# Performance work log

Measured on AMD Instinct MI355X. Metric: run time of the kernel, lower is better.

Reference implementation:

```python
import jax, jax.numpy as jnp
import numpy as np

H = 16
DH = 64  # n_state // n_head = 1024 // 16
EPS = 1e-6


def phi(x):
    return jax.nn.silu(x) + 1.0


def setup_inputs() -> dict:
    key = jax.random.key(0)
    ks = jax.random.split(key, 9)
    B, C, Tq, Tk = 8, 1024, 1500, 1500
    s = 1.0 / np.sqrt(C).astype(np.float32)
    return {
        "x": jax.random.normal(ks[0], (B, C, Tq, 1), jnp.float32),
        "xa": jax.random.normal(ks[1], (B, C, Tk, 1), jnp.float32),
        "Wq": jax.random.normal(ks[2], (C, C), jnp.float32) * s,
        "bq": jax.random.normal(ks[3], (C,), jnp.float32) * s,
        "Wk": jax.random.normal(ks[4], (C, C), jnp.float32) * s,
        "Wv": jax.random.normal(ks[5], (C, C), jnp.float32) * s,
        "bv": jax.random.normal(ks[6], (C,), jnp.float32) * s,
        "Wo": jax.random.normal(ks[7], (C, C), jnp.float32) * s,
        "bo": jax.random.normal(ks[8], (C,), jnp.float32) * s,
    }


def reference(x, xa, Wq, bq, Wk, Wv, bv, Wo, bo):
    # x: (B,C,Tq,1), xa: (B,C,Tk,1). 1x1 conv2d == matmul over channel dim.
    xq = x[..., 0]   # (B,C,Tq)
    xk = xa[..., 0]  # (B,C,Tk)
    q = jnp.einsum('oc,bct->bot', Wq, xq) + bq[None, :, None]
    k = jnp.einsum('oc,bct->bot', Wk, xk)  # key has no bias
    v = jnp.einsum('oc,bct->bot', Wv, xk) + bv[None, :, None]

    B, C, Tq = q.shape
    Tk = k.shape[2]
    pq = phi(q).reshape(B, H, DH, Tq)
    pk = phi(k).reshape(B, H, DH, Tk)
    vv = v.reshape(B, H, DH, Tk)

    k_sum = pk.sum(axis=3)            # (B,H,Dh) : sum_t phi(k)
    kv_sum = (pk * vv).sum(axis=3)    # (B,H,Dh) : diagonal phi(k)*v sum (as in source)
    den = jnp.einsum('bhdt,bhd->bht', pq, k_sum) + EPS  # (B,H,Tq)

    out = pq * kv_sum[..., None] / den[:, :, None, :]   # (B,H,Dh,Tq)
    out = out.reshape(B, C, Tq) / jnp.sqrt(jnp.asarray(DH, out.dtype))
    y = jnp.einsum('oc,bct->bot', Wo, out) + bo[None, :, None]
    return y[..., None]  # (B,C,Tq,1)
```

## Files before the change

### kernel.cpp

```cpp
#include <hip/hip_runtime.h>

typedef __attribute__((ext_vector_type(4))) float  f32x4;
typedef __attribute__((ext_vector_type(4))) float  float4v;
typedef __attribute__((ext_vector_type(8))) short  short8;
typedef __attribute__((ext_vector_type(4))) short  short4v;

#define TQ 1500
#define TP 1536
#define CC 1024
#define EPS 1e-6f

#define XT_OFF    ((size_t)0)
#define XAT_OFF   ((size_t)25165824)
#define PQT_OFF   ((size_t)50331648)
#define WB_OFF    ((size_t)75497472)
#define KSUM_OFF  ((size_t)83886080)
#define KVSUM_OFF ((size_t)83918848)
#define IDEN_OFF  ((size_t)83951616)

__device__ __forceinline__ float bf2f(short s) {
    union { unsigned u; float f; } v; v.u = ((unsigned)(unsigned short)s) << 16; return v.f;
}
__device__ __forceinline__ short f2bf(float f) {
    union { float f; unsigned u; } v; v.f = f;
    unsigned r = (v.u + 0x7FFFu + ((v.u >> 16) & 1u)) >> 16;
    return (short)r;
}
__device__ __forceinline__ float phi_f(float x) {
    return x / (1.f + __expf(-x)) + 1.f;
}
__device__ __forceinline__ void gl_lds16(const void* g, void* l) {
    __builtin_amdgcn_global_load_lds((const __attribute__((address_space(1))) void*)g,
                                     (__attribute__((address_space(3))) void*)l, 16, 0, 0);
}

__global__ __launch_bounds__(256)
void conv_w_kernel(const float* __restrict__ w0, const float* __restrict__ w1,
                   const float* __restrict__ w2, const float* __restrict__ w3,
                   short* __restrict__ o0, short* __restrict__ o1,
                   short* __restrict__ o2, short* __restrict__ o3)
{
    const int i = (blockIdx.x * 256 + threadIdx.x) * 4;
    float4v a = *(const float4v*)(w0 + i);
    float4v b = *(const float4v*)(w1 + i);
    float4v c = *(const float4v*)(w2 + i);
    float4v d = *(const float4v*)(w3 + i);
    short4v ra, rb, rc, rd;
#pragma unroll
    for (int j = 0; j < 4; ++j) {
        ra[j] = f2bf(a[j]); rb[j] = f2bf(b[j]); rc[j] = f2bf(c[j]); rd[j] = f2bf(d[j]);
    }
    *(short4v*)(o0 + i) = ra;
    *(short4v*)(o1 + i) = rb;
    *(short4v*)(o2 + i) = rc;
    *(short4v*)(o3 + i) = rd;
}

__global__ __launch_bounds__(256)
void xpose_kernel(const float* __restrict__ x, short* __restrict__ xT)
{
    __shared__ float tile[64][65];
    const int b  = blockIdx.z;
    const int c0 = blockIdx.y * 64;
    const int t0 = blockIdx.x * 64;
    const int tl = threadIdx.x & 63;
    const int q  = threadIdx.x >> 6;
    const int t  = t0 + tl;
#pragma unroll
    for (int i = 0; i < 16; ++i) {
        const int cl = q * 16 + i;
        float v = 0.f;
        if (t < TQ) v = x[((size_t)b * CC + c0 + cl) * TQ + t];
        tile[cl][tl] = v;
    }
    __syncthreads();
#pragma unroll
    for (int i = 0; i < 16; ++i) {
        const int t2 = q * 16 + i;
        xT[((size_t)b * TP + t0 + t2) * CC + c0 + tl] = f2bf(tile[tl][t2]);
    }
}

__global__ __launch_bounds__(256)
void gemm_q_kernel(const short* __restrict__ xT, const short* __restrict__ Wqb,
                   const float* __restrict__ bq, short* __restrict__ pqT)
{
    __shared__ short As[128 * 32];
    __shared__ short Bs[128 * 32];
    const int b    = blockIdx.z;
    const int mt   = blockIdx.y;
    const int nt   = blockIdx.x;
    const int tid  = threadIdx.x;
    const int wave = tid >> 6, lane = tid & 63;
    const int wr = wave >> 1, wc = wave & 1;
    const int srow = lane >> 2;
    const int skof = (lane & 3) << 3;
    const int rl   = lane & 15;
    const int rg   = (lane >> 4) << 3;
    const int rgrp = lane >> 4;

    const short* Ab = xT + (size_t)b * TP * CC + (size_t)mt * 128 * CC;
    const short* Bb = Wqb + (size_t)nt * 128 * CC;

    f32x4 acc[4][4] = {};

    for (int kt = 0; kt < CC / 32; ++kt) {
        const int k0 = kt << 5;
#pragma unroll
        for (int c2 = 0; c2 < 2; ++c2) {
            const int ch = wave * 2 + c2;
            gl_lds16(Ab + (size_t)(ch * 16 + srow) * CC + k0 + skof, &As[ch * 512]);
            gl_lds16(Bb + (size_t)(ch * 16 + srow) * CC + k0 + skof, &Bs[ch * 512]);
        }
        __syncthreads();
        short8 ra[4], rb[4];
#pragma unroll
        for (int i = 0; i < 4; ++i) {
            ra[i] = *(const short8*)&As[(wr * 64 + i * 16 + rl) * 32 + rg];
            rb[i] = *(const short8*)&Bs[(wc * 64 + i * 16 + rl) * 32 + rg];
        }
#pragma unroll
        for (int i = 0; i < 4; ++i)
#pragma unroll
            for (int j = 0; j < 4; ++j)
                acc[i][j] = __builtin_amdgcn_mfma_f32_16x16x32_bf16(ra[i], rb[j], acc[i][j], 0, 0, 0);
        __syncthreads();
    }

#pragma unroll
    for (int j = 0; j < 4; ++j) {
        const int c = nt * 128 + wc * 64 + j * 16 + rl;
        const float bias = bq[c];
#pragma unroll
        for (int i = 0; i < 4; ++i) {
            const int tbase = mt * 128 + wr * 64 + i * 16 + rgrp * 4;
#pragma unroll
            for (int r = 0; r < 4; ++r) {
                float v = acc[i][j][r] + bias;
                pqT[((size_t)b * TP + tbase + r) * CC + c] = f2bf(phi_f(v));
            }
        }
    }
}

__global__ __launch_bounds__(256)
void gemm_kv_kernel(const short* __restrict__ xaT, const short* __restrict__ Wkb,
                    const short* __restrict__ Wvb, const float* __restrict__ bv,
                    float* __restrict__ ksum, float* __restrict__ kvsum)
{
    __shared__ short As[128 * 32];
    __shared__ short Bks[64 * 32];
    __shared__ short Bvs[64 * 32];
    const int b    = blockIdx.z;
    const int mt   = blockIdx.y;
    const int nt   = blockIdx.x;
    const int tid  = threadIdx.x;
    const int wave = tid >> 6, lane = tid & 63;
    const int wr = wave >> 1, wc = wave & 1;
    const int srow = lane >> 2;
    const int skof = (lane & 3) << 3;
    const int rl   = lane & 15;
    const int rg   = (lane >> 4) << 3;
    const int rgrp = lane >> 4;

    const short* Ab  = xaT + (size_t)b * TP * CC + (size_t)mt * 128 * CC;
    const short* Bkb = Wkb + (size_t)nt * 64 * CC;
    const short* Bvb = Wvb + (size_t)nt * 64 * CC;

    f32x4 ak[4][2] = {};
    f32x4 av[4][2] = {};

    for (int kt = 0; kt < CC / 32; ++kt) {
        const int k0 = kt << 5;
#pragma unroll
        for (int c2 = 0; c2 < 2; ++c2) {
            const int ch = wave * 2 + c2;
            gl_lds16(Ab + (size_t)(ch * 16 + srow) * CC + k0 + skof, &As[ch * 512]);
        }
        gl_lds16(Bkb + (size_t)(wave * 16 + srow) * CC + k0 + skof, &Bks[wave * 512]);
        gl_lds16(Bvb + (size_t)(wave * 16 + srow) * CC + k0 + skof, &Bvs[wave * 512]);
        __syncthreads();
        short8 ra[4], rk[2], rv[2];
#pragma unroll
        for (int i = 0; i < 4; ++i)
            ra[i] = *(const short8*)&As[(wr * 64 + i * 16 + rl) * 32 + rg];
#pragma unroll
        for (int j = 0; j < 2; ++j) {
            rk[j] = *(const short8*)&Bks[(wc * 32 + j * 16 + rl) * 32 + rg];
            rv[j] = *(const short8*)&Bvs[(wc * 32 + j * 16 + rl) * 32 + rg];
        }
#pragma unroll
        for (int i = 0; i < 4; ++i)
#pragma unroll
            for (int j = 0; j < 2; ++j) {
                ak[i][j] = __builtin_amdgcn_mfma_f32_16x16x32_bf16(ra[i], rk[j], ak[i][j], 0, 0, 0);
                av[i][j] = __builtin_amdgcn_mfma_f32_16x16x32_bf16(ra[i], rv[j], av[i][j], 0, 0, 0);
            }
        __syncthreads();
    }

#pragma unroll
    for (int j = 0; j < 2; ++j) {
        const int c = nt * 64 + wc * 32 + j * 16 + rl;
        const float bvc = bv[c];
        float sk = 0.f, skv = 0.f;
#pragma unroll
        for (int i = 0; i < 4; ++i) {
            const int tbase = mt * 128 + wr * 64 + i * 16 + rgrp * 4;
#pragma unroll
            for (int r = 0; r < 4; ++r) {
                if (tbase + r < TQ) {
                    float pk = phi_f(ak[i][j][r]);
                    float vv = av[i][j][r] + bvc;
                    sk  += pk;
                    skv += pk * vv;
                }
            }
        }
        sk  += __shfl_xor(sk, 16);  sk  += __shfl_xor(sk, 32);
        skv += __shfl_xor(skv, 16); skv += __shfl_xor(skv, 32);
        if (rgrp == 0) {
            atomicAdd(&ksum[b * CC + c], sk);
            atomicAdd(&kvsum[b * CC + c], skv);
        }
    }
}

__global__ __launch_bounds__(64)
void den_kernel(const short* __restrict__ pqT, const float* __restrict__ ksum,
                float* __restrict__ invden)
{
    const int b = blockIdx.z, h = blockIdx.y;
    const int t = blockIdx.x * 64 + threadIdx.x;
    const short* row = pqT + ((size_t)b * TP + t) * CC + h * 64;
    const float* ks  = ksum + b * CC + h * 64;
    float s = 0.f;
#pragma unroll
    for (int i = 0; i < 8; ++i) {
        short8 p = *(const short8*)&row[i * 8];
#pragma unroll
        for (int j = 0; j < 8; ++j)
            s += bf2f(p[j]) * ks[i * 8 + j];
    }
    invden[((size_t)b * 16 + h) * TP + t] = 0.125f / (s + EPS);
}

__global__ __launch_bounds__(128)
void out_kernel(const short* __restrict__ pqT, const float* __restrict__ kvsum,
                const float* __restrict__ invden, short* __restrict__ outT)
{
    const int t = blockIdx.x, b = blockIdx.y;
    const int c0 = threadIdx.x * 8;
    const size_t base = ((size_t)b * TP + t) * CC + c0;
    short8 p = *(const short8*)(pqT + base);
    const float id = invden[((size_t)b * 16 + (c0 >> 6)) * TP + t];
    const float* kv = kvsum + b * CC + c0;
    short8 o;
#pragma unroll
    for (int j = 0; j < 8; ++j)
        o[j] = f2bf(bf2f(p[j]) * kv[j] * id);
    *(short8*)(outT + base) = o;
}

__global__ __launch_bounds__(256)
void gemm_o_kernel(const short* __restrict__ Wob, const short* __restrict__ outT,
                   const float* __restrict__ bo, float* __restrict__ y)
{
    __shared__ short As[128 * 32];
    __shared__ short Bs[128 * 32];
    const int b    = blockIdx.z;
    const int ct   = blockIdx.y;
    const int tt   = blockIdx.x;
    const int tid  = threadIdx.x;
    const int wave = tid >> 6, lane = tid & 63;
    const int wr = wave >> 1, wc = wave & 1;
    const int srow = lane >> 2;
    const int skof = (lane & 3) << 3;
    const int rl   = lane & 15;
    const int rg   = (lane >> 4) << 3;
    const int rgrp = lane >> 4;

    const short* Ab = Wob + (size_t)ct * 128 * CC;
    const short* Bb = outT + (size_t)b * TP * CC + (size_t)tt * 128 * CC;

    f32x4 acc[4][4] = {};

    for (int kt = 0; kt < CC / 32; ++kt) {
        const int k0 = kt << 5;
#pragma unroll
        for (int c2 = 0; c2 < 2; ++c2) {
            const int ch = wave * 2 + c2;
            gl_lds16(Ab + (size_t)(ch * 16 + srow) * CC + k0 + skof, &As[ch * 512]);
            gl_lds16(Bb + (size_t)(ch * 16 + srow) * CC + k0 + skof, &Bs[ch * 512]);
        }
        __syncthreads();
        short8 ra[4], rb[4];
#pragma unroll
        for (int i = 0; i < 4; ++i) {
            ra[i] = *(const short8*)&As[(wr * 64 + i * 16 + rl) * 32 + rg];
            rb[i] = *(const short8*)&Bs[(wc * 64 + i * 16 + rl) * 32 + rg];
        }
#pragma unroll
        for (int i = 0; i < 4; ++i)
#pragma unroll
            for (int j = 0; j < 4; ++j)
                acc[i][j] = __builtin_amdgcn_mfma_f32_16x16x32_bf16(ra[i], rb[j], acc[i][j], 0, 0, 0);
        __syncthreads();
    }

#pragma unroll
    for (int j = 0; j < 4; ++j) {
        const int tcol = tt * 128 + wc * 64 + j * 16 + rl;
        if (tcol >= TQ) continue;
#pragma unroll
        for (int i = 0; i < 4; ++i) {
            const int cbase = ct * 128 + wr * 64 + i * 16 + rgrp * 4;
#pragma unroll
            for (int r = 0; r < 4; ++r) {
                const int c = cbase + r;
                y[((size_t)b * CC + c) * TQ + tcol] = acc[i][j][r] + bo[c];
            }
        }
    }
}

extern "C" void kernel_launch(void* const* d_in, const int* in_sizes, int n_in,
                              void* d_out, int out_size, void* d_ws, size_t ws_size,
                              hipStream_t stream)
{
    (void)in_sizes; (void)n_in; (void)out_size; (void)ws_size;
    const float* x  = (const float*)d_in[0];
    const float* xa = (const float*)d_in[1];
    const float* Wq = (const float*)d_in[2];
    const float* bq = (const float*)d_in[3];
    const float* Wk = (const float*)d_in[4];
    const float* Wv = (const float*)d_in[5];
    const float* bv = (const float*)d_in[6];
    const float* Wo = (const float*)d_in[7];
    const float* bo = (const float*)d_in[8];
    float* y = (float*)d_out;
    char* ws = (char*)d_ws;

    short* xT    = (short*)(ws + XT_OFF);
    short* xaT   = (short*)(ws + XAT_OFF);
    short* pqT   = (short*)(ws + PQT_OFF);
    short* Wqb   = (short*)(ws + WB_OFF);
    short* Wkb   = Wqb + (size_t)CC * CC;
    short* Wvb   = Wkb + (size_t)CC * CC;
    short* Wob   = Wvb + (size_t)CC * CC;
    float* ksum  = (float*)(ws + KSUM_OFF);
    float* kvsum = (float*)(ws + KVSUM_OFF);
    float* iden  = (float*)(ws + IDEN_OFF);
    short* outT  = xT;

    conv_w_kernel<<<dim3(CC * CC / 4 / 256), 256, 0, stream>>>(Wq, Wk, Wv, Wo, Wqb, Wkb, Wvb, Wob);
    xpose_kernel<<<dim3(TP / 64, CC / 64, 8), 256, 0, stream>>>(x, xT);
    xpose_kernel<<<dim3(TP / 64, CC / 64, 8), 256, 0, stream>>>(xa, xaT);
    hipMemsetAsync(ws + KSUM_OFF, 0, 65536, stream);

    gemm_kv_kernel<<<dim3(CC / 64, TP / 128, 8), 256, 0, stream>>>(xaT, Wkb, Wvb, bv, ksum, kvsum);
    gemm_q_kernel<<<dim3(CC / 128, TP / 128, 8), 256, 0, stream>>>(xT, Wqb, bq, pqT);
    den_kernel<<<dim3(TP / 64, 16, 8), 64, 0, stream>>>(pqT, ksum, iden);
    out_kernel<<<dim3(TP, 8), 128, 0, stream>>>(pqT, kvsum, iden, outT);
    gemm_o_kernel<<<dim3(TP / 128, CC / 128, 8), 256, 0, stream>>>(Wob, outT, bo, y);
}
```

Before: 384.6 us.

## Fuse denominator and output scaling into Q GEMM epilogue; swizzle LDS, remap blocks

The phi(q), per-head denominator and kv_sum scaling are now computed in the Q GEMM epilogue. Each wave already holds one head's 64 channels, so the denominator is reduced with lane shuffles, and the separate den and out kernels plus the pqT round trip through global memory disappear. The two transpose launches are merged into one grid, and all GEMMs use a 1D grid remapped so consecutive blocks are spread across XCDs, aiming for better L2 locality. LDS tiles get an XOR swizzle on the k-chunk to reduce bank conflicts on reads. The cost is a longer epilogue with more registers and shuffles in the Q GEMM.

```diff
diff --git a/kernel.cpp b/kernel.cpp
--- a/kernel.cpp
+++ b/kernel.cpp
@@ -12,11 +12,10 @@
 
 #define XT_OFF    ((size_t)0)
 #define XAT_OFF   ((size_t)25165824)
-#define PQT_OFF   ((size_t)50331648)
+#define OUT_OFF   ((size_t)50331648)
 #define WB_OFF    ((size_t)75497472)
 #define KSUM_OFF  ((size_t)83886080)
 #define KVSUM_OFF ((size_t)83918848)
-#define IDEN_OFF  ((size_t)83951616)
 
 __device__ __forceinline__ float bf2f(short s) {
     union { unsigned u; float f; } v; v.u = ((unsigned)(unsigned short)s) << 16; return v.f;
@@ -33,6 +32,7 @@
     __builtin_amdgcn_global_load_lds((const __attribute__((address_space(1))) void*)g,
                                      (__attribute__((address_space(3))) void*)l, 16, 0, 0);
 }
+
 
 __global__ __launch_bounds__(256)
 void conv_w_kernel(const float* __restrict__ w0, const float* __restrict__ w1,
@@ -57,10 +57,14 @@
 }
 
 __global__ __launch_bounds__(256)
-void xpose_kernel(const float* __restrict__ x, short* __restrict__ xT)
+void xpose_kernel(const float* __restrict__ x, const float* __restrict__ xa,
+                  short* __restrict__ xT, short* __restrict__ xaT)
 {
     __shared__ float tile[64][65];
-    const int b  = blockIdx.z;
+    const int z  = blockIdx.z;
+    const int b  = z & 7;
+    const float* src = (z < 8) ? x : xa;
+    short* dst       = (z < 8) ? xT : xaT;
     const int c0 = blockIdx.y * 64;
     const int t0 = blockIdx.x * 64;
     const int tl = threadIdx.x & 63;
@@ -70,97 +74,37 @@
     for (int i = 0; i < 16; ++i) {
         const int cl = q * 16 + i;
         float v = 0.f;
-        if (t < TQ) v = x[((size_t)b * CC + c0 + cl) * TQ + t];
+        if (t < TQ) v = src[((size_t)b * CC + c0 + cl) * TQ + t];
         tile[cl][tl] = v;
     }
     __syncthreads();
 #pragma unroll
     for (int i = 0; i < 16; ++i) {
         const int t2 = q * 16 + i;
-        xT[((size_t)b * TP + t0 + t2) * CC + c0 + tl] = f2bf(tile[tl][t2]);
-    }
-}
-
-__global__ __launch_bounds__(256)
-void gemm_q_kernel(const short* __restrict__ xT, const short* __restrict__ Wqb,
-                   const float* __restrict__ bq, short* __restrict__ pqT)
+        dst[((size_t)b * TP + t0 + t2) * CC + c0 + tl] = f2bf(tile[tl][t2]);
+    }
+}
+
+__global__ __launch_bounds__(256)
+void gemm_kv_kernel(const short* __restrict__ xaT, const short* __restrict__ Wkb,
+                    const short* __restrict__ Wvb, const float* __restrict__ bv,
+                    float* __restrict__ ksum, float* __restrict__ kvsum)
 {
     __shared__ short As[128 * 32];
-    __shared__ short Bs[128 * 32];
-    const int b    = blockIdx.z;
-    const int mt   = blockIdx.y;
-    const int nt   = blockIdx.x;
+    __shared__ short Bks[64 * 32];
+    __shared__ short Bvs[64 * 32];
+    const int f  = blockIdx.x;
+    const int L  = (f & 7) * 192 + (f >> 3);
+    const int nt = L % 16;
+    const int mt = (L / 16) % 12;
+    const int b  = L / 192;
     const int tid  = threadIdx.x;
     const int wave = tid >> 6, lane = tid & 63;
     const int wr = wave >> 1, wc = wave & 1;
     const int srow = lane >> 2;
-    const int skof = (lane & 3) << 3;
+    const int skof = (((lane & 3) ^ ((srow >> 1) & 3)) << 3);
     const int rl   = lane & 15;
-    const int rg   = (lane >> 4) << 3;
-    const int rgrp = lane >> 4;
-
-    const short* Ab = xT + (size_t)b * TP * CC + (size_t)mt * 128 * CC;
-    const short* Bb = Wqb + (size_t)nt * 128 * CC;
-
-    f32x4 acc[4][4] = {};
-
-    for (int kt = 0; kt < CC / 32; ++kt) {
-        const int k0 = kt << 5;
-#pragma unroll
-        for (int c2 = 0; c2 < 2; ++c2) {
-            const int ch = wave * 2 + c2;
-            gl_lds16(Ab + (size_t)(ch * 16 + srow) * CC + k0 + skof, &As[ch * 512]);
-            gl_lds16(Bb + (size_t)(ch * 16 + srow) * CC + k0 + skof, &Bs[ch * 512]);
-        }
-        __syncthreads();
-        short8 ra[4], rb[4];
-#pragma unroll
-        for (int i = 0; i < 4; ++i) {
-            ra[i] = *(const short8*)&As[(wr * 64 + i * 16 + rl) * 32 + rg];
-            rb[i] = *(const short8*)&Bs[(wc * 64 + i * 16 + rl) * 32 + rg];
-        }
-#pragma unroll
-        for (int i = 0; i < 4; ++i)
-#pragma unroll
-            for (int j = 0; j < 4; ++j)
-                acc[i][j] = __builtin_amdgcn_mfma_f32_16x16x32_bf16(ra[i], rb[j], acc[i][j], 0, 0, 0);
-        __syncthreads();
-    }
-
-#pragma unroll
-    for (int j = 0; j < 4; ++j) {
-        const int c = nt * 128 + wc * 64 + j * 16 + rl;
-        const float bias = bq[c];
-#pragma unroll
-        for (int i = 0; i < 4; ++i) {
-            const int tbase = mt * 128 + wr * 64 + i * 16 + rgrp * 4;
-#pragma unroll
-            for (int r = 0; r < 4; ++r) {
-                float v = acc[i][j][r] + bias;
-                pqT[((size_t)b * TP + tbase + r) * CC + c] = f2bf(phi_f(v));
-            }
-        }
-    }
-}
-
-__global__ __launch_bounds__(256)
-void gemm_kv_kernel(const short* __restrict__ xaT, const short* __restrict__ Wkb,
-                    const short* __restrict__ Wvb, const float* __restrict__ bv,
-                    float* __restrict__ ksum, float* __restrict__ kvsum)
-{
-    __shared__ short As[128 * 32];
-    __shared__ short Bks[64 * 32];
-    __shared__ short Bvs[64 * 32];
-    const int b    = blockIdx.z;
-    const int mt   = blockIdx.y;
-    const int nt   = blockIdx.x;
-    const int tid  = threadIdx.x;
-    const int wave = tid >> 6, lane = tid & 63;
-    const int wr = wave >> 1, wc = wave & 1;
-    const int srow = lane >> 2;
-    const int skof = (lane & 3) << 3;
-    const int rl   = lane & 15;
-    const int rg   = (lane >> 4) << 3;
+    const int rg   = ((((lane >> 4)) ^ ((rl >> 1) & 3)) << 3);
     const int rgrp = lane >> 4;
 
     const short* Ab  = xaT + (size_t)b * TP * CC + (size_t)mt * 128 * CC;
@@ -226,58 +170,107 @@
     }
 }
 
-__global__ __launch_bounds__(64)
-void den_kernel(const short* __restrict__ pqT, const float* __restrict__ ksum,
-                float* __restrict__ invden)
-{
-    const int b = blockIdx.z, h = blockIdx.y;
-    const int t = blockIdx.x * 64 + threadIdx.x;
-    const short* row = pqT + ((size_t)b * TP + t) * CC + h * 64;
-    const float* ks  = ksum + b * CC + h * 64;
-    float s = 0.f;
-#pragma unroll
-    for (int i = 0; i < 8; ++i) {
-        short8 p = *(const short8*)&row[i * 8];
-#pragma unroll
-        for (int j = 0; j < 8; ++j)
-            s += bf2f(p[j]) * ks[i * 8 + j];
-    }
-    invden[((size_t)b * 16 + h) * TP + t] = 0.125f / (s + EPS);
-}
-
-__global__ __launch_bounds__(128)
-void out_kernel(const short* __restrict__ pqT, const float* __restrict__ kvsum,
-                const float* __restrict__ invden, short* __restrict__ outT)
-{
-    const int t = blockIdx.x, b = blockIdx.y;
-    const int c0 = threadIdx.x * 8;
-    const size_t base = ((size_t)b * TP + t) * CC + c0;
-    short8 p = *(const short8*)(pqT + base);
-    const float id = invden[((size_t)b * 16 + (c0 >> 6)) * TP + t];
-    const float* kv = kvsum + b * CC + c0;
-    short8 o;
-#pragma unroll
-    for (int j = 0; j < 8; ++j)
-        o[j] = f2bf(bf2f(p[j]) * kv[j] * id);
-    *(short8*)(outT + base) = o;
-}
-
-__global__ __launch_bounds__(256)
-void gemm_o_kernel(const short* __restrict__ Wob, const short* __restrict__ outT,
-                   const float* __restrict__ bo, float* __restrict__ y)
+__global__ __launch_bounds__(256)
+void gemm_q_out_kernel(const short* __restrict__ xT, const short* __restrict__ Wqb,
+                       const float* __restrict__ bq, const float* __restrict__ ksum,
+                       const float* __restrict__ kvsum, short* __restrict__ outT)
 {
     __shared__ short As[128 * 32];
     __shared__ short Bs[128 * 32];
-    const int b    = blockIdx.z;
-    const int ct   = blockIdx.y;
-    const int tt   = blockIdx.x;
+    const int f  = blockIdx.x;
+    const int L  = (f & 7) * 96 + (f >> 3);
+    const int nt = L % 8;
+    const int mt = (L / 8) % 12;
+    const int b  = L / 96;
     const int tid  = threadIdx.x;
     const int wave = tid >> 6, lane = tid & 63;
     const int wr = wave >> 1, wc = wave & 1;
     const int srow = lane >> 2;
-    const int skof = (lane & 3) << 3;
+    const int skof = (((lane & 3) ^ ((srow >> 1) & 3)) << 3);
     const int rl   = lane & 15;
-    const int rg   = (lane >> 4) << 3;
+    const int rg   = ((((lane >> 4)) ^ ((rl >> 1) & 3)) << 3);
+    const int rgrp = lane >> 4;
+
+    const short* Ab = xT + (size_t)b * TP * CC + (size_t)mt * 128 * CC;
+    const short* Bb = Wqb + (size_t)nt * 128 * CC;
+
+    f32x4 acc[4][4] = {};
+
+    for (int kt = 0; kt < CC / 32; ++kt) {
+        const int k0 = kt << 5;
+#pragma unroll
+        for (int c2 = 0; c2 < 2; ++c2) {
+            const int ch = wave * 2 + c2;
+            gl_lds16(Ab + (size_t)(ch * 16 + srow) * CC + k0 + skof, &As[ch * 512]);
+            gl_lds16(Bb + (size_t)(ch * 16 + srow) * CC + k0 + skof, &Bs[ch * 512]);
+        }
+        __syncthreads();
+        short8 ra[4], rb[4];
+#pragma unroll
+        for (int i = 0; i < 4; ++i) {
+            ra[i] = *(const short8*)&As[(wr * 64 + i * 16 + rl) * 32 + rg];
+            rb[i] = *(const short8*)&Bs[(wc * 64 + i * 16 + rl) * 32 + rg];
+        }
+#pragma unroll
+        for (int i = 0; i < 4; ++i)
+#pragma unroll
+            for (int j = 0; j < 4; ++j)
+                acc[i][j] = __builtin_amdgcn_mfma_f32_16x16x32_bf16(ra[i], rb[j], acc[i][j], 0, 0, 0);
+        __syncthreads();
+    }
+
+    float bias[4], ks[4], kv[4];
+#pragma unroll
+    for (int j = 0; j < 4; ++j) {
+        const int c = nt * 128 + wc * 64 + j * 16 + rl;
+        bias[j] = bq[c];
+        ks[j]   = ksum[b * CC + c];
+        kv[j]   = kvsum[b * CC + c];
+    }
+#pragma unroll
+    for (int i = 0; i < 4; ++i)
+#pragma unroll
+        for (int j = 0; j < 4; ++j)
+#pragma unroll
+            for (int r = 0; r < 4; ++r)
+                acc[i][j][r] = phi_f(acc[i][j][r] + bias[j]);
+#pragma unroll
+    for (int i = 0; i < 4; ++i) {
+#pragma unroll
+        for (int r = 0; r < 4; ++r) {
+            float d = acc[i][0][r] * ks[0] + acc[i][1][r] * ks[1]
+                    + acc[i][2][r] * ks[2] + acc[i][3][r] * ks[3];
+            d += __shfl_xor(d, 1); d += __shfl_xor(d, 2);
+            d += __shfl_xor(d, 4); d += __shfl_xor(d, 8);
+            const float inv = 0.125f / (d + EPS);
+            const int t = mt * 128 + wr * 64 + i * 16 + rgrp * 4 + r;
+#pragma unroll
+            for (int j = 0; j < 4; ++j) {
+                const int c = nt * 128 + wc * 64 + j * 16 + rl;
+                outT[((size_t)b * TP + t) * CC + c] = f2bf(acc[i][j][r] * kv[j] * inv);
+            }
+        }
+    }
+}
+
+__global__ __launch_bounds__(256)
+void gemm_o_kernel(const short* __restrict__ Wob, const short* __restrict__ outT,
+                   const float* __restrict__ bo, float* __restrict__ y)
+{
+    __shared__ short As[128 * 32];
+    __shared__ short Bs[128 * 32];
+    const int f  = blockIdx.x;
+    const int L  = (f & 7) * 96 + (f >> 3);
+    const int tt = L % 12;
+    const int ct = (L / 12) % 8;
+    const int b  = L / 96;
+    const int tid  = threadIdx.x;
+    const int wave = tid >> 6, lane = tid & 63;
+    const int wr = wave >> 1, wc = wave & 1;
+    const int srow = lane >> 2;
+    const int skof = (((lane & 3) ^ ((srow >> 1) & 3)) << 3);
+    const int rl   = lane & 15;
+    const int rg   = ((((lane >> 4)) ^ ((rl >> 1) & 3)) << 3);
     const int rgrp = lane >> 4;
 
     const short* Ab = Wob + (size_t)ct * 128 * CC;
@@ -343,24 +336,19 @@
 
     short* xT    = (short*)(ws + XT_OFF);
     short* xaT   = (short*)(ws + XAT_OFF);
-    short* pqT   = (short*)(ws + PQT_OFF);
+    short* outT  = (short*)(ws + OUT_OFF);
     short* Wqb   = (short*)(ws + WB_OFF);
     short* Wkb   = Wqb + (size_t)CC * CC;
     short* Wvb   = Wkb + (size_t)CC * CC;
     short* Wob   = Wvb + (size_t)CC * CC;
     float* ksum  = (float*)(ws + KSUM_OFF);
     float* kvsum = (float*)(ws + KVSUM_OFF);
-    float* iden  = (float*)(ws + IDEN_OFF);
-    short* outT  = xT;
 
     conv_w_kernel<<<dim3(CC * CC / 4 / 256), 256, 0, stream>>>(Wq, Wk, Wv, Wo, Wqb, Wkb, Wvb, Wob);
-    xpose_kernel<<<dim3(TP / 64, CC / 64, 8), 256, 0, stream>>>(x, xT);
-    xpose_kernel<<<dim3(TP / 64, CC / 64, 8), 256, 0, stream>>>(xa, xaT);
+    xpose_kernel<<<dim3(TP / 64, CC / 64, 16), 256, 0, stream>>>(x, xa, xT, xaT);
     hipMemsetAsync(ws + KSUM_OFF, 0, 65536, stream);
 
-    gemm_kv_kernel<<<dim3(CC / 64, TP / 128, 8), 256, 0, stream>>>(xaT, Wkb, Wvb, bv, ksum, kvsum);
-    gemm_q_kernel<<<dim3(CC / 128, TP / 128, 8), 256, 0, stream>>>(xT, Wqb, bq, pqT);
-    den_kernel<<<dim3(TP / 64, 16, 8), 64, 0, stream>>>(pqT, ksum, iden);
-    out_kernel<<<dim3(TP, 8), 128, 0, stream>>>(pqT, kvsum, iden, outT);
-    gemm_o_kernel<<<dim3(TP / 128, CC / 128, 8), 256, 0, stream>>>(Wob, outT, bo, y);
-}
+    gemm_kv_kernel<<<dim3(1536), 256, 0, stream>>>(xaT, Wkb, Wvb, bv, ksum, kvsum);
+    gemm_q_out_kernel<<<dim3(768), 256, 0, stream>>>(xT, Wqb, bq, ksum, kvsum, outT);
+    gemm_o_kernel<<<dim3(768), 256, 0, stream>>>(Wob, outT, bo, y);
+}
```

Result: faster. 358.7 us (-6.8%).
